# Performance work log

Hardware: AMD Instinct MI355X
Metric: run time of the kernel (lower is better)

The kernel has to match this reference:

```python
import jax, jax.numpy as jnp
import numpy as np

B, S_NEW, DIM = 32, 1, 4096
H, KV, HD = 32, 8, 128          # query heads, kv heads, head_dim
PREV = 2048                      # tokens already in the KV cache


def setup_inputs() -> dict:
    key = jax.random.key(0)
    ks = jax.random.split(key, 8)
    return {
        "x": jax.random.normal(ks[0], (B, S_NEW, DIM), jnp.float32),
        "wq": jax.random.normal(ks[1], (DIM, H * HD), jnp.float32) * 0.02,
        "wk": jax.random.normal(ks[2], (DIM, KV * HD), jnp.float32) * 0.02,
        "wv": jax.random.normal(ks[3], (DIM, KV * HD), jnp.float32) * 0.02,
        "wo": jax.random.normal(ks[4], (H * HD, DIM), jnp.float32) * 0.02,
        "cache_k": jax.random.normal(ks[5], (B, PREV, KV, HD), jnp.float32),
        "cache_v": jax.random.normal(ks[6], (B, PREV, KV, HD), jnp.float32),
        "freqs": jax.random.normal(ks[7], (S_NEW, HD // 2), jnp.float32),  # rotary angles (angle of freqs_cis)
    }


def _apply_rope(t, cos, sin):
    # t: [b, s, h, hd]; interleaved pairs as in torch.view_as_complex
    a = t[..., 0::2]
    b = t[..., 1::2]
    c = cos[None, :, None, :]
    s = sin[None, :, None, :]
    ra = a * c - b * s
    rb = a * s + b * c
    return jnp.stack([ra, rb], axis=-1).reshape(t.shape)


def reference(x, wq, wk, wv, wo, cache_k, cache_v, freqs):
    b, s, _ = x.shape  # s == 1 (decode)
    xq = (x @ wq).reshape(b, s, H, HD)
    xk = (x @ wk).reshape(b, s, KV, HD)
    xv = (x @ wv).reshape(b, s, KV, HD)

    cos, sin = jnp.cos(freqs), jnp.sin(freqs)
    xq = _apply_rope(xq, cos, sin)
    xk = _apply_rope(xk, cos, sin)

    # KV-cache append (update_cache_decode)
    k_full = jnp.concatenate([cache_k, xk], axis=1)  # [b, PREV+1, KV, hd]
    v_full = jnp.concatenate([cache_v, xv], axis=1)

    # GQA attention without materializing the expanded cache
    g = H // KV
    q = xq.reshape(b, KV, g, HD)  # s == 1 folded away
    scale = 1.0 / jnp.sqrt(jnp.asarray(HD, x.dtype))
    scores = jnp.einsum("bkgd,bskd->bkgs", q, k_full) * scale  # [b, KV, g, PREV+1]
    attn = jax.nn.softmax(scores, axis=-1)
    out = jnp.einsum("bkgs,bskd->bkgd", attn, v_full)  # [b, KV, g, hd]
    out = out.reshape(b, s, H * HD)
    return out @ wo
```

## Files before the change

kernel.cpp:

```cpp
#include <hip/hip_runtime.h>


#define WS_P1   0
#define WS_QKV  6291456
#define WS_ATTN 6488064
#define WS_P2   6619136
#define WS_SC   10813440
#define WS_LINV 12914688
#define WS_PA   12915712

__global__ __launch_bounds__(256) void gemm_skinny(
    const float* __restrict__ X,
    const float* __restrict__ W0, int e0, int ld0,
    const float* __restrict__ W1, int e1, int ld1,
    const float* __restrict__ W2, int ld2,
    float* __restrict__ P, int Ntot)
{
    __shared__ float x_t[128][36];
    __shared__ float2 red[128][33];

    const int nb = blockIdx.x * 256;
    const float* W; int ld, noff;
    if (nb < e0)      { W = W0; ld = ld0; noff = 0;  }
    else if (nb < e1) { W = W1; ld = ld1; noff = e0; }
    else              { W = W2; ld = ld2; noff = e1; }

    const int k0  = blockIdx.y * 128;
    const int tid = threadIdx.x;
    const int cp  = tid & 127;
    const int kg  = tid >> 7;
    const int nn  = nb - noff + cp * 2;

    #pragma unroll
    for (int i = 0; i < 16; ++i) {
        int idx = tid + i * 256;
        int bb = idx >> 7, kk = idx & 127;
        x_t[kk][bb] = X[(size_t)bb * 4096 + k0 + kk];
    }
    __syncthreads();

    float2 acc[32];
    #pragma unroll
    for (int b = 0; b < 32; ++b) { acc[b].x = 0.f; acc[b].y = 0.f; }

    const float* Wp = W + (size_t)k0 * ld + nn;
    for (int kk0 = kg * 64; kk0 < kg * 64 + 64; kk0 += 8) {
        float2 w[8];
        #pragma unroll
        for (int u = 0; u < 8; ++u)
            w[u] = *(const float2*)&Wp[(size_t)(kk0 + u) * ld];
        #pragma unroll
        for (int u = 0; u < 8; ++u) {
            const float* xr = x_t[kk0 + u];
            #pragma unroll
            for (int bq = 0; bq < 8; ++bq) {
                float4 xv = *(const float4*)&xr[bq * 4];
                acc[bq*4+0].x += xv.x * w[u].x; acc[bq*4+0].y += xv.x * w[u].y;
                acc[bq*4+1].x += xv.y * w[u].x; acc[bq*4+1].y += xv.y * w[u].y;
                acc[bq*4+2].x += xv.z * w[u].x; acc[bq*4+2].y += xv.z * w[u].y;
                acc[bq*4+3].x += xv.w * w[u].x; acc[bq*4+3].y += xv.w * w[u].y;
            }
        }
    }

    if (kg == 1) {
        #pragma unroll
        for (int b = 0; b < 32; ++b) red[cp][b] = acc[b];
    }
    __syncthreads();
    if (kg == 0) {
        const int ks = blockIdx.y;
        #pragma unroll
        for (int b = 0; b < 32; ++b) {
            float2 o = red[cp][b];
            float2 v; v.x = acc[b].x + o.x; v.y = acc[b].y + o.y;
            *(float2*)&P[((size_t)ks * 32 + b) * Ntot + nb + cp * 2] = v;
        }
    }
}

__global__ __launch_bounds__(128) void reduce_rope(
    const float* __restrict__ P, const float* __restrict__ freqs,
    float* __restrict__ qkv)
{
    int t = blockIdx.x * 128 + threadIdx.x;
    int b = t / 3072;
    int cp = t - b * 3072;
    int n = cp * 2;
    float sx = 0.f, sy = 0.f;
    #pragma unroll
    for (int ks = 0; ks < 32; ++ks) {
        float2 v = *(const float2*)&P[((size_t)ks * 32 + b) * 6144 + n];
        sx += v.x; sy += v.y;
    }
    if (n < 5120) {
        int d = n & 127;
        float fr = freqs[d >> 1];
        float c = cosf(fr), s = sinf(fr);
        float ra = sx * c - sy * s;
        float rb = sx * s + sy * c;
        if (n < 4096) {
            const float sc = 0.08838834764831845f;
            ra *= sc; rb *= sc;
        }
        sx = ra; sy = rb;
    }
    float2 o; o.x = sx; o.y = sy;
    *(float2*)&qkv[(size_t)b * 6144 + n] = o;
}

__global__ __launch_bounds__(256) void attn_scores(
    const float* __restrict__ qkv,
    const float* __restrict__ ck,
    float* __restrict__ sc)
{
    const int blk = blockIdx.x;
    const int c   = blk & 15;
    const int kv  = (blk >> 4) & 7;
    const int b   = blk >> 7;
    const int tid = threadIdx.x;
    const int wave = tid >> 6, lane = tid & 63;
    const int psub = (lane >> 4) & 3, dl = lane & 15;
    const int s0 = c * 128;

    float q[4][8];
    {
        const float* qb = qkv + (size_t)b * 6144 + kv * 512 + dl * 8;
        #pragma unroll
        for (int h = 0; h < 4; ++h) {
            float4 a = *(const float4*)&qb[h * 128];
            float4 e = *(const float4*)&qb[h * 128 + 4];
            q[h][0]=a.x; q[h][1]=a.y; q[h][2]=a.z; q[h][3]=a.w;
            q[h][4]=e.x; q[h][5]=e.y; q[h][6]=e.z; q[h][7]=e.w;
        }
    }

    float* scb = sc + (size_t)(b * 8 + kv) * 8208;
    const float* kbase = ck + (((size_t)b * 2048 + s0) * 8 + kv) * 128;
    const int srow = wave * 4 + psub;

    for (int it0 = 0; it0 < 8; it0 += 2) {
        float4 kA[2][2];
        #pragma unroll
        for (int u = 0; u < 2; ++u) {
            const float* kr = kbase + (size_t)((it0 + u) * 16 + srow) * 1024 + dl * 8;
            kA[u][0] = *(const float4*)kr;
            kA[u][1] = *(const float4*)(kr + 4);
        }
        #pragma unroll
        for (int u = 0; u < 2; ++u) {
            float p[4];
            #pragma unroll
            for (int h = 0; h < 4; ++h) {
                p[h] = q[h][0]*kA[u][0].x + q[h][1]*kA[u][0].y
                     + q[h][2]*kA[u][0].z + q[h][3]*kA[u][0].w
                     + q[h][4]*kA[u][1].x + q[h][5]*kA[u][1].y
                     + q[h][6]*kA[u][1].z + q[h][7]*kA[u][1].w;
            }
            #pragma unroll
            for (int off = 1; off < 16; off <<= 1) {
                #pragma unroll
                for (int h = 0; h < 4; ++h) p[h] += __shfl_xor(p[h], off);
            }
            if (dl == 0) {
                int s = s0 + (it0 + u) * 16 + srow;
                float4 o; o.x = p[0]; o.y = p[1]; o.z = p[2]; o.w = p[3];
                *(float4*)&scb[(size_t)s * 4] = o;
            }
        }
    }

    if (c == 15 && wave == 0 && psub == 0) {
        const float* kr = qkv + (size_t)b * 6144 + 4096 + kv * 128 + dl * 8;
        float4 k0 = *(const float4*)kr;
        float4 k1 = *(const float4*)(kr + 4);
        float p[4];
        #pragma unroll
        for (int h = 0; h < 4; ++h) {
            p[h] = q[h][0]*k0.x + q[h][1]*k0.y + q[h][2]*k0.z + q[h][3]*k0.w
                 + q[h][4]*k1.x + q[h][5]*k1.y + q[h][6]*k1.z + q[h][7]*k1.w;
        }
        #pragma unroll
        for (int off = 1; off < 16; off <<= 1) {
            #pragma unroll
            for (int h = 0; h < 4; ++h) p[h] += __shfl_xor(p[h], off);
        }
        if (dl == 0) {
            float4 o; o.x = p[0]; o.y = p[1]; o.z = p[2]; o.w = p[3];
            *(float4*)&scb[(size_t)2048 * 4] = o;
        }
    }
}

__global__ __launch_bounds__(256) void attn_softmax(
    float* __restrict__ sc, float* __restrict__ linv)
{
    __shared__ float red[4][4];
    const int g = blockIdx.x;
    float* scb = sc + (size_t)g * 8208;
    const int tid = threadIdx.x;
    const int wave = tid >> 6, lane = tid & 63;

    float4 m4; m4.x = -1e30f; m4.y = -1e30f; m4.z = -1e30f; m4.w = -1e30f;
    for (int s = tid; s < 2049; s += 256) {
        float4 v = *(const float4*)&scb[(size_t)s * 4];
        m4.x = fmaxf(m4.x, v.x); m4.y = fmaxf(m4.y, v.y);
        m4.z = fmaxf(m4.z, v.z); m4.w = fmaxf(m4.w, v.w);
    }
    #pragma unroll
    for (int off = 1; off < 64; off <<= 1) {
        m4.x = fmaxf(m4.x, __shfl_xor(m4.x, off));
        m4.y = fmaxf(m4.y, __shfl_xor(m4.y, off));
        m4.z = fmaxf(m4.z, __shfl_xor(m4.z, off));
        m4.w = fmaxf(m4.w, __shfl_xor(m4.w, off));
    }
    if (lane == 0) {
        red[wave][0] = m4.x; red[wave][1] = m4.y;
        red[wave][2] = m4.z; red[wave][3] = m4.w;
    }
    __syncthreads();
    float4 M;
    M.x = fmaxf(fmaxf(red[0][0], red[1][0]), fmaxf(red[2][0], red[3][0]));
    M.y = fmaxf(fmaxf(red[0][1], red[1][1]), fmaxf(red[2][1], red[3][1]));
    M.z = fmaxf(fmaxf(red[0][2], red[1][2]), fmaxf(red[2][2], red[3][2]));
    M.w = fmaxf(fmaxf(red[0][3], red[1][3]), fmaxf(red[2][3], red[3][3]));
    __syncthreads();

    float4 l4; l4.x = 0.f; l4.y = 0.f; l4.z = 0.f; l4.w = 0.f;
    for (int s = tid; s < 2049; s += 256) {
        float4 v = *(const float4*)&scb[(size_t)s * 4];
        v.x = __expf(v.x - M.x); v.y = __expf(v.y - M.y);
        v.z = __expf(v.z - M.z); v.w = __expf(v.w - M.w);
        *(float4*)&scb[(size_t)s * 4] = v;
        l4.x += v.x; l4.y += v.y; l4.z += v.z; l4.w += v.w;
    }
    #pragma unroll
    for (int off = 1; off < 64; off <<= 1) {
        l4.x += __shfl_xor(l4.x, off);
        l4.y += __shfl_xor(l4.y, off);
        l4.z += __shfl_xor(l4.z, off);
        l4.w += __shfl_xor(l4.w, off);
    }
    if (lane == 0) {
        red[wave][0] = l4.x; red[wave][1] = l4.y;
        red[wave][2] = l4.z; red[wave][3] = l4.w;
    }
    __syncthreads();
    if (tid < 4) {
        float L = red[0][tid] + red[1][tid] + red[2][tid] + red[3][tid];
        linv[(size_t)g * 4 + tid] = 1.0f / L;
    }
}

__global__ __launch_bounds__(256) void attn_pv(
    const float* __restrict__ qkv, const float* __restrict__ cv,
    const float* __restrict__ sc, const float* __restrict__ linv,
    float* __restrict__ pa)
{
    __shared__ float sbuf[8][512];
    const int blk = blockIdx.x;
    const int c   = blk & 7;
    const int kv  = (blk >> 3) & 7;
    const int b   = blk >> 6;
    const int tid = threadIdx.x;
    const int grp = tid >> 5, l32 = tid & 31, d4 = l32 * 4;
    const int s0 = c * 256;

    const float* scb = sc + (size_t)(b * 8 + kv) * 8208;
    const float* vbase = cv + (((size_t)b * 2048 + s0) * 8 + kv) * 128;

    float4 acc[4];
    #pragma unroll
    for (int h = 0; h < 4; ++h) { acc[h].x=0.f; acc[h].y=0.f; acc[h].z=0.f; acc[h].w=0.f; }

    for (int it = 0; it < 8; ++it) {
        float4 vv[4];
        float4 pj[4];
        #pragma unroll
        for (int j = 0; j < 4; ++j) {
            int sl = it * 32 + j * 8 + grp;
            vv[j] = *(const float4*)&vbase[(size_t)sl * 1024 + d4];
        }
        #pragma unroll
        for (int j = 0; j < 4; ++j) {
            int sl = it * 32 + j * 8 + grp;
            pj[j] = *(const float4*)&scb[(size_t)(s0 + sl) * 4];
        }
        #pragma unroll
        for (int j = 0; j < 4; ++j) {
            acc[0].x += pj[j].x * vv[j].x; acc[0].y += pj[j].x * vv[j].y;
            acc[0].z += pj[j].x * vv[j].z; acc[0].w += pj[j].x * vv[j].w;
            acc[1].x += pj[j].y * vv[j].x; acc[1].y += pj[j].y * vv[j].y;
            acc[1].z += pj[j].y * vv[j].z; acc[1].w += pj[j].y * vv[j].w;
            acc[2].x += pj[j].z * vv[j].x; acc[2].y += pj[j].z * vv[j].y;
            acc[2].z += pj[j].z * vv[j].z; acc[2].w += pj[j].z * vv[j].w;
            acc[3].x += pj[j].w * vv[j].x; acc[3].y += pj[j].w * vv[j].y;
            acc[3].z += pj[j].w * vv[j].z; acc[3].w += pj[j].w * vv[j].w;
        }
    }
    if (c == 7 && grp == 0) {
        const float* vr = qkv + (size_t)b * 6144 + 5120 + kv * 128;
        float4 v = *(const float4*)&vr[d4];
        float4 p = *(const float4*)&scb[(size_t)2048 * 4];
        acc[0].x += p.x * v.x; acc[0].y += p.x * v.y; acc[0].z += p.x * v.z; acc[0].w += p.x * v.w;
        acc[1].x += p.y * v.x; acc[1].y += p.y * v.y; acc[1].z += p.y * v.z; acc[1].w += p.y * v.w;
        acc[2].x += p.z * v.x; acc[2].y += p.z * v.y; acc[2].z += p.z * v.z; acc[2].w += p.z * v.w;
        acc[3].x += p.w * v.x; acc[3].y += p.w * v.y; acc[3].z += p.w * v.z; acc[3].w += p.w * v.w;
    }

    {
        float4 li = *(const float4*)&linv[(size_t)(b * 8 + kv) * 4];
        acc[0].x *= li.x; acc[0].y *= li.x; acc[0].z *= li.x; acc[0].w *= li.x;
        acc[1].x *= li.y; acc[1].y *= li.y; acc[1].z *= li.y; acc[1].w *= li.y;
        acc[2].x *= li.z; acc[2].y *= li.z; acc[2].z *= li.z; acc[2].w *= li.z;
        acc[3].x *= li.w; acc[3].y *= li.w; acc[3].z *= li.w; acc[3].w *= li.w;
    }
    #pragma unroll
    for (int h = 0; h < 4; ++h)
        *(float4*)&sbuf[grp][h * 128 + d4] = acc[h];
    __syncthreads();

    float* rec = pa + (size_t)blk * 512;
    for (int t = tid; t < 512; t += 256) {
        float v = 0.f;
        #pragma unroll
        for (int g2 = 0; g2 < 8; ++g2) v += sbuf[g2][t];
        rec[t] = v;
    }
}

__global__ __launch_bounds__(128) void attn_combine(
    const float* __restrict__ pa, float* __restrict__ ao)
{
    const int g = blockIdx.x;
    const int d = threadIdx.x;
    const float* base = pa + (size_t)g * 8 * 512;
    #pragma unroll
    for (int h = 0; h < 4; ++h) {
        float v = 0.f;
        #pragma unroll
        for (int c = 0; c < 8; ++c) v += base[c * 512 + h * 128 + d];
        ao[(size_t)(g >> 3) * 4096 + (g & 7) * 512 + h * 128 + d] = v;
    }
}

__global__ __launch_bounds__(128) void reduce_out(
    const float* __restrict__ P, float* __restrict__ out)
{
    int t = blockIdx.x * 128 + threadIdx.x;
    int b = t >> 11;
    int cp = t & 2047;
    int n = cp * 2;
    float sx = 0.f, sy = 0.f;
    #pragma unroll
    for (int ks = 0; ks < 32; ++ks) {
        float2 v = *(const float2*)&P[((size_t)ks * 32 + b) * 4096 + n];
        sx += v.x; sy += v.y;
    }
    float2 o; o.x = sx; o.y = sy;
    *(float2*)&out[(size_t)b * 4096 + n] = o;
}

extern "C" void kernel_launch(void* const* d_in, const int* in_sizes, int n_in,
                              void* d_out, int out_size, void* d_ws, size_t ws_size,
                              hipStream_t stream) {
    const float* x  = (const float*)d_in[0];
    const float* wq = (const float*)d_in[1];
    const float* wk = (const float*)d_in[2];
    const float* wv = (const float*)d_in[3];
    const float* wo = (const float*)d_in[4];
    const float* ck = (const float*)d_in[5];
    const float* cv = (const float*)d_in[6];
    const float* fr = (const float*)d_in[7];
    float* out = (float*)d_out;
    float* ws  = (float*)d_ws;

    float* P1   = ws + WS_P1;
    float* qkv  = ws + WS_QKV;
    float* attn = ws + WS_ATTN;
    float* P2   = ws + WS_P2;
    float* SC   = ws + WS_SC;
    float* LINV = ws + WS_LINV;
    float* PA   = ws + WS_PA;

    dim3 g1(24, 32);
    gemm_skinny<<<g1, 256, 0, stream>>>(x, wq, 4096, 4096, wk, 5120, 1024,
                                        wv, 1024, P1, 6144);
    reduce_rope<<<768, 128, 0, stream>>>(P1, fr, qkv);
    attn_scores<<<4096, 256, 0, stream>>>(qkv, ck, SC);
    attn_softmax<<<256, 256, 0, stream>>>(SC, LINV);
    attn_pv<<<2048, 256, 0, stream>>>(qkv, cv, SC, LINV, PA);
    attn_combine<<<256, 128, 0, stream>>>(PA, attn);
    dim3 g4(16, 32);
    gemm_skinny<<<g4, 256, 0, stream>>>(attn, wo, 4096, 4096, wo, 4096, 4096,
                                        wo, 4096, P2, 4096);
    reduce_out<<<512, 128, 0, stream>>>(P2, out);
}
```

Baseline: 207.3 us.

## Cover all KV heads per block in attention scores and PV over contiguous rows

attn_scores and attn_pv now give each block 32 contiguous sequence rows across all 8 KV heads, instead of one KV head over a longer span. Each block therefore streams full 4 KB cache rows contiguously. The score buffer becomes a per-batch interleaved [s][kv][4] layout, and softmax is adapted to read it. The PV partials grow to 64 chunks of 4096 floats per batch, and a rewritten combine kernel reduces them. This adds extra workspace traffic and footprint in exchange for more contiguous cache reads.

Measured after the change: 247.3 us. +19.3%, slower.

```diff
diff --git a/kernel.cpp b/kernel.cpp
--- a/kernel.cpp
+++ b/kernel.cpp
@@ -110,84 +110,78 @@
 }
 
 __global__ __launch_bounds__(256) void attn_scores(
-    const float* __restrict__ qkv,
-    const float* __restrict__ ck,
+    const float* __restrict__ qkv, const float* __restrict__ ck,
     float* __restrict__ sc)
 {
     const int blk = blockIdx.x;
-    const int c   = blk & 15;
-    const int kv  = (blk >> 4) & 7;
-    const int b   = blk >> 7;
-    const int tid = threadIdx.x;
-    const int wave = tid >> 6, lane = tid & 63;
-    const int psub = (lane >> 4) & 3, dl = lane & 15;
-    const int s0 = c * 128;
-
-    float q[4][8];
+    const int c = blk & 63;
+    const int b = blk >> 6;
+    const int t = threadIdx.x;
+    const int jj = t & 15;
+    const int kv = (t >> 4) & 7;
+    const int tm = t >> 7;
+
+    float4 q[4][2];
     {
-        const float* qb = qkv + (size_t)b * 6144 + kv * 512 + dl * 8;
+        const float* qb = qkv + (size_t)b * 6144 + (kv * 4) * 128 + jj * 8;
         #pragma unroll
         for (int h = 0; h < 4; ++h) {
-            float4 a = *(const float4*)&qb[h * 128];
-            float4 e = *(const float4*)&qb[h * 128 + 4];
-            q[h][0]=a.x; q[h][1]=a.y; q[h][2]=a.z; q[h][3]=a.w;
-            q[h][4]=e.x; q[h][5]=e.y; q[h][6]=e.z; q[h][7]=e.w;
-        }
-    }
-
-    float* scb = sc + (size_t)(b * 8 + kv) * 8208;
-    const float* kbase = ck + (((size_t)b * 2048 + s0) * 8 + kv) * 128;
-    const int srow = wave * 4 + psub;
-
-    for (int it0 = 0; it0 < 8; it0 += 2) {
-        float4 kA[2][2];
+            q[h][0] = *(const float4*)(qb + h * 128);
+            q[h][1] = *(const float4*)(qb + h * 128 + 4);
+        }
+    }
+
+    const int r0 = c * 32 + tm * 16;
+    const float* kbase = ck + ((size_t)b * 2048 + r0) * 1024 + kv * 128 + jj * 8;
+    float* scb = sc + (size_t)b * 65664;
+
+    for (int r = 0; r < 16; r += 2) {
+        float4 ka[2][2];
         #pragma unroll
         for (int u = 0; u < 2; ++u) {
-            const float* kr = kbase + (size_t)((it0 + u) * 16 + srow) * 1024 + dl * 8;
-            kA[u][0] = *(const float4*)kr;
-            kA[u][1] = *(const float4*)(kr + 4);
+            ka[u][0] = *(const float4*)(kbase + (size_t)(r + u) * 1024);
+            ka[u][1] = *(const float4*)(kbase + (size_t)(r + u) * 1024 + 4);
         }
         #pragma unroll
         for (int u = 0; u < 2; ++u) {
             float p[4];
             #pragma unroll
             for (int h = 0; h < 4; ++h) {
-                p[h] = q[h][0]*kA[u][0].x + q[h][1]*kA[u][0].y
-                     + q[h][2]*kA[u][0].z + q[h][3]*kA[u][0].w
-                     + q[h][4]*kA[u][1].x + q[h][5]*kA[u][1].y
-                     + q[h][6]*kA[u][1].z + q[h][7]*kA[u][1].w;
+                p[h] = q[h][0].x*ka[u][0].x + q[h][0].y*ka[u][0].y
+                     + q[h][0].z*ka[u][0].z + q[h][0].w*ka[u][0].w
+                     + q[h][1].x*ka[u][1].x + q[h][1].y*ka[u][1].y
+                     + q[h][1].z*ka[u][1].z + q[h][1].w*ka[u][1].w;
             }
             #pragma unroll
             for (int off = 1; off < 16; off <<= 1) {
                 #pragma unroll
                 for (int h = 0; h < 4; ++h) p[h] += __shfl_xor(p[h], off);
             }
-            if (dl == 0) {
-                int s = s0 + (it0 + u) * 16 + srow;
+            if (jj == 0) {
                 float4 o; o.x = p[0]; o.y = p[1]; o.z = p[2]; o.w = p[3];
-                *(float4*)&scb[(size_t)s * 4] = o;
+                *(float4*)&scb[(size_t)(r0 + r + u) * 32 + kv * 4] = o;
             }
         }
     }
 
-    if (c == 15 && wave == 0 && psub == 0) {
-        const float* kr = qkv + (size_t)b * 6144 + 4096 + kv * 128 + dl * 8;
+    if (c == 63 && tm == 1) {
+        const float* kr = qkv + (size_t)b * 6144 + 4096 + kv * 128 + jj * 8;
         float4 k0 = *(const float4*)kr;
         float4 k1 = *(const float4*)(kr + 4);
         float p[4];
         #pragma unroll
         for (int h = 0; h < 4; ++h) {
-            p[h] = q[h][0]*k0.x + q[h][1]*k0.y + q[h][2]*k0.z + q[h][3]*k0.w
-                 + q[h][4]*k1.x + q[h][5]*k1.y + q[h][6]*k1.z + q[h][7]*k1.w;
+            p[h] = q[h][0].x*k0.x + q[h][0].y*k0.y + q[h][0].z*k0.z + q[h][0].w*k0.w
+                 + q[h][1].x*k1.x + q[h][1].y*k1.y + q[h][1].z*k1.z + q[h][1].w*k1.w;
         }
         #pragma unroll
         for (int off = 1; off < 16; off <<= 1) {
             #pragma unroll
             for (int h = 0; h < 4; ++h) p[h] += __shfl_xor(p[h], off);
         }
-        if (dl == 0) {
+        if (jj == 0) {
             float4 o; o.x = p[0]; o.y = p[1]; o.z = p[2]; o.w = p[3];
-            *(float4*)&scb[(size_t)2048 * 4] = o;
+            *(float4*)&scb[(size_t)2048 * 32 + kv * 4] = o;
         }
     }
 }
@@ -197,13 +191,14 @@
 {
     __shared__ float red[4][4];
     const int g = blockIdx.x;
-    float* scb = sc + (size_t)g * 8208;
+    const int b = g >> 3, kv = g & 7;
+    float* scb = sc + (size_t)b * 65664 + kv * 4;
     const int tid = threadIdx.x;
     const int wave = tid >> 6, lane = tid & 63;
 
     float4 m4; m4.x = -1e30f; m4.y = -1e30f; m4.z = -1e30f; m4.w = -1e30f;
     for (int s = tid; s < 2049; s += 256) {
-        float4 v = *(const float4*)&scb[(size_t)s * 4];
+        float4 v = *(const float4*)&scb[(size_t)s * 32];
         m4.x = fmaxf(m4.x, v.x); m4.y = fmaxf(m4.y, v.y);
         m4.z = fmaxf(m4.z, v.z); m4.w = fmaxf(m4.w, v.w);
     }
@@ -228,10 +223,10 @@
 
     float4 l4; l4.x = 0.f; l4.y = 0.f; l4.z = 0.f; l4.w = 0.f;
     for (int s = tid; s < 2049; s += 256) {
-        float4 v = *(const float4*)&scb[(size_t)s * 4];
+        float4 v = *(const float4*)&scb[(size_t)s * 32];
         v.x = __expf(v.x - M.x); v.y = __expf(v.y - M.y);
         v.z = __expf(v.z - M.z); v.w = __expf(v.w - M.w);
-        *(float4*)&scb[(size_t)s * 4] = v;
+        *(float4*)&scb[(size_t)s * 32] = v;
         l4.x += v.x; l4.y += v.y; l4.z += v.z; l4.w += v.w;
     }
     #pragma unroll
@@ -257,91 +252,123 @@
     const float* __restrict__ sc, const float* __restrict__ linv,
     float* __restrict__ pa)
 {
-    __shared__ float sbuf[8][512];
+    __shared__ float sbuf[128 * 33];
     const int blk = blockIdx.x;
-    const int c   = blk & 7;
-    const int kv  = (blk >> 3) & 7;
-    const int b   = blk >> 6;
-    const int tid = threadIdx.x;
-    const int grp = tid >> 5, l32 = tid & 31, d4 = l32 * 4;
-    const int s0 = c * 256;
-
-    const float* scb = sc + (size_t)(b * 8 + kv) * 8208;
-    const float* vbase = cv + (((size_t)b * 2048 + s0) * 8 + kv) * 128;
-
-    float4 acc[4];
-    #pragma unroll
-    for (int h = 0; h < 4; ++h) { acc[h].x=0.f; acc[h].y=0.f; acc[h].z=0.f; acc[h].w=0.f; }
-
-    for (int it = 0; it < 8; ++it) {
-        float4 vv[4];
-        float4 pj[4];
-        #pragma unroll
-        for (int j = 0; j < 4; ++j) {
-            int sl = it * 32 + j * 8 + grp;
-            vv[j] = *(const float4*)&vbase[(size_t)sl * 1024 + d4];
-        }
-        #pragma unroll
-        for (int j = 0; j < 4; ++j) {
-            int sl = it * 32 + j * 8 + grp;
-            pj[j] = *(const float4*)&scb[(size_t)(s0 + sl) * 4];
-        }
-        #pragma unroll
-        for (int j = 0; j < 4; ++j) {
-            acc[0].x += pj[j].x * vv[j].x; acc[0].y += pj[j].x * vv[j].y;
-            acc[0].z += pj[j].x * vv[j].z; acc[0].w += pj[j].x * vv[j].w;
-            acc[1].x += pj[j].y * vv[j].x; acc[1].y += pj[j].y * vv[j].y;
-            acc[1].z += pj[j].y * vv[j].z; acc[1].w += pj[j].y * vv[j].w;
-            acc[2].x += pj[j].z * vv[j].x; acc[2].y += pj[j].z * vv[j].y;
-            acc[2].z += pj[j].z * vv[j].z; acc[2].w += pj[j].z * vv[j].w;
-            acc[3].x += pj[j].w * vv[j].x; acc[3].y += pj[j].w * vv[j].y;
-            acc[3].z += pj[j].w * vv[j].z; acc[3].w += pj[j].w * vv[j].w;
-        }
-    }
-    if (c == 7 && grp == 0) {
-        const float* vr = qkv + (size_t)b * 6144 + 5120 + kv * 128;
-        float4 v = *(const float4*)&vr[d4];
-        float4 p = *(const float4*)&scb[(size_t)2048 * 4];
-        acc[0].x += p.x * v.x; acc[0].y += p.x * v.y; acc[0].z += p.x * v.z; acc[0].w += p.x * v.w;
-        acc[1].x += p.y * v.x; acc[1].y += p.y * v.y; acc[1].z += p.y * v.z; acc[1].w += p.y * v.w;
-        acc[2].x += p.z * v.x; acc[2].y += p.z * v.y; acc[2].z += p.z * v.z; acc[2].w += p.z * v.w;
-        acc[3].x += p.w * v.x; acc[3].y += p.w * v.y; acc[3].z += p.w * v.z; acc[3].w += p.w * v.w;
+    const int c = blk & 63;
+    const int b = blk >> 6;
+    const int t = threadIdx.x;
+    const int jj = t & 15;
+    const int kv = (t >> 4) & 7;
+    const int tm = t >> 7;
+
+    float4 acc[4][2];
+    #pragma unroll
+    for (int h = 0; h < 4; ++h) {
+        #pragma unroll
+        for (int u = 0; u < 2; ++u) { acc[h][u].x=0.f; acc[h][u].y=0.f; acc[h][u].z=0.f; acc[h][u].w=0.f; }
+    }
+
+    const int r0 = c * 32 + tm * 16;
+    const float* vbase = cv + ((size_t)b * 2048 + r0) * 1024 + kv * 128 + jj * 8;
+    const float* scb = sc + (size_t)b * 65664 + kv * 4;
+
+    for (int r = 0; r < 16; r += 2) {
+        float4 va[2][2];
+        float4 p4[2];
+        #pragma unroll
+        for (int u = 0; u < 2; ++u) {
+            va[u][0] = *(const float4*)(vbase + (size_t)(r + u) * 1024);
+            va[u][1] = *(const float4*)(vbase + (size_t)(r + u) * 1024 + 4);
+            p4[u] = *(const float4*)&scb[(size_t)(r0 + r + u) * 32];
+        }
+        #pragma unroll
+        for (int u = 0; u < 2; ++u) {
+            acc[0][0].x += p4[u].x*va[u][0].x; acc[0][0].y += p4[u].x*va[u][0].y;
+            acc[0][0].z += p4[u].x*va[u][0].z; acc[0][0].w += p4[u].x*va[u][0].w;
+            acc[0][1].x += p4[u].x*va[u][1].x; acc[0][1].y += p4[u].x*va[u][1].y;
+            acc[0][1].z += p4[u].x*va[u][1].z; acc[0][1].w += p4[u].x*va[u][1].w;
+            acc[1][0].x += p4[u].y*va[u][0].x; acc[1][0].y += p4[u].y*va[u][0].y;
+            acc[1][0].z += p4[u].y*va[u][0].z; acc[1][0].w += p4[u].y*va[u][0].w;
+            acc[1][1].x += p4[u].y*va[u][1].x; acc[1][1].y += p4[u].y*va[u][1].y;
+            acc[1][1].z += p4[u].y*va[u][1].z; acc[1][1].w += p4[u].y*va[u][1].w;
+            acc[2][0].x += p4[u].z*va[u][0].x; acc[2][0].y += p4[u].z*va[u][0].y;
+            acc[2][0].z += p4[u].z*va[u][0].z; acc[2][0].w += p4[u].z*va[u][0].w;
+            acc[2][1].x += p4[u].z*va[u][1].x; acc[2][1].y += p4[u].z*va[u][1].y;
+            acc[2][1].z += p4[u].z*va[u][1].z; acc[2][1].w += p4[u].z*va[u][1].w;
+            acc[3][0].x += p4[u].w*va[u][0].x; acc[3][0].y += p4[u].w*va[u][0].y;
+            acc[3][0].z += p4[u].w*va[u][0].z; acc[3][0].w += p4[u].w*va[u][0].w;
+            acc[3][1].x += p4[u].w*va[u][1].x; acc[3][1].y += p4[u].w*va[u][1].y;
+            acc[3][1].z += p4[u].w*va[u][1].z; acc[3][1].w += p4[u].w*va[u][1].w;
+        }
+    }
+
+    if (c == 63 && tm == 1) {
+        const float* vr = qkv + (size_t)b * 6144 + 5120 + kv * 128 + jj * 8;
+        float4 v0 = *(const float4*)vr;
+        float4 v1 = *(const float4*)(vr + 4);
+        float4 p = *(const float4*)&scb[(size_t)2048 * 32];
+        acc[0][0].x += p.x*v0.x; acc[0][0].y += p.x*v0.y; acc[0][0].z += p.x*v0.z; acc[0][0].w += p.x*v0.w;
+        acc[0][1].x += p.x*v1.x; acc[0][1].y += p.x*v1.y; acc[0][1].z += p.x*v1.z; acc[0][1].w += p.x*v1.w;
+        acc[1][0].x += p.y*v0.x; acc[1][0].y += p.y*v0.y; acc[1][0].z += p.y*v0.z; acc[1][0].w += p.y*v0.w;
+        acc[1][1].x += p.y*v1.x; acc[1][1].y += p.y*v1.y; acc[1][1].z += p.y*v1.z; acc[1][1].w += p.y*v1.w;
+        acc[2][0].x += p.z*v0.x; acc[2][0].y += p.z*v0.y; acc[2][0].z += p.z*v0.z; acc[2][0].w += p.z*v0.w;
+        acc[2][1].x += p.z*v1.x; acc[2][1].y += p.z*v1.y; acc[2][1].z += p.z*v1.z; acc[2][1].w += p.z*v1.w;
+        acc[3][0].x += p.w*v0.x; acc[3][0].y += p.w*v0.y; acc[3][0].z += p.w*v0.z; acc[3][0].w += p.w*v0.w;
+        acc[3][1].x += p.w*v1.x; acc[3][1].y += p.w*v1.y; acc[3][1].z += p.w*v1.z; acc[3][1].w += p.w*v1.w;
     }
 
     {
-        float4 li = *(const float4*)&linv[(size_t)(b * 8 + kv) * 4];
-        acc[0].x *= li.x; acc[0].y *= li.x; acc[0].z *= li.x; acc[0].w *= li.x;
-        acc[1].x *= li.y; acc[1].y *= li.y; acc[1].z *= li.y; acc[1].w *= li.y;
-        acc[2].x *= li.z; acc[2].y *= li.z; acc[2].z *= li.z; acc[2].w *= li.z;
-        acc[3].x *= li.w; acc[3].y *= li.w; acc[3].z *= li.w; acc[3].w *= li.w;
-    }
-    #pragma unroll
-    for (int h = 0; h < 4; ++h)
-        *(float4*)&sbuf[grp][h * 128 + d4] = acc[h];
-    __syncthreads();
-
-    float* rec = pa + (size_t)blk * 512;
-    for (int t = tid; t < 512; t += 256) {
-        float v = 0.f;
-        #pragma unroll
-        for (int g2 = 0; g2 < 8; ++g2) v += sbuf[g2][t];
-        rec[t] = v;
-    }
-}
-
-__global__ __launch_bounds__(128) void attn_combine(
+        float4 li = *(const float4*)&linv[(size_t)((b * 8 + kv) * 4)];
+        #pragma unroll
+        for (int u = 0; u < 2; ++u) {
+            acc[0][u].x *= li.x; acc[0][u].y *= li.x; acc[0][u].z *= li.x; acc[0][u].w *= li.x;
+            acc[1][u].x *= li.y; acc[1][u].y *= li.y; acc[1][u].z *= li.y; acc[1][u].w *= li.y;
+            acc[2][u].x *= li.z; acc[2][u].y *= li.z; acc[2][u].z *= li.z; acc[2][u].w *= li.z;
+            acc[3][u].x *= li.w; acc[3][u].y *= li.w; acc[3][u].z *= li.w; acc[3][u].w *= li.w;
+        }
+    }
+
+    if (tm == 1) {
+        const int li_ = t - 128;
+        float* d = &sbuf[li_ * 33];
+        #pragma unroll
+        for (int h = 0; h < 4; ++h) {
+            d[h*8+0] = acc[h][0].x; d[h*8+1] = acc[h][0].y;
+            d[h*8+2] = acc[h][0].z; d[h*8+3] = acc[h][0].w;
+            d[h*8+4] = acc[h][1].x; d[h*8+5] = acc[h][1].y;
+            d[h*8+6] = acc[h][1].z; d[h*8+7] = acc[h][1].w;
+        }
+    }
+    __syncthreads();
+    if (tm == 0) {
+        const float* s_ = &sbuf[t * 33];
+        #pragma unroll
+        for (int h = 0; h < 4; ++h) {
+            acc[h][0].x += s_[h*8+0]; acc[h][0].y += s_[h*8+1];
+            acc[h][0].z += s_[h*8+2]; acc[h][0].w += s_[h*8+3];
+            acc[h][1].x += s_[h*8+4]; acc[h][1].y += s_[h*8+5];
+            acc[h][1].z += s_[h*8+6]; acc[h][1].w += s_[h*8+7];
+        }
+        float* rec = pa + (size_t)blk * 4096 + (kv * 4) * 128 + jj * 8;
+        #pragma unroll
+        for (int h = 0; h < 4; ++h) {
+            *(float4*)(rec + h * 128)     = acc[h][0];
+            *(float4*)(rec + h * 128 + 4) = acc[h][1];
+        }
+    }
+}
+
+__global__ __launch_bounds__(256) void attn_combine(
     const float* __restrict__ pa, float* __restrict__ ao)
 {
-    const int g = blockIdx.x;
-    const int d = threadIdx.x;
-    const float* base = pa + (size_t)g * 8 * 512;
-    #pragma unroll
-    for (int h = 0; h < 4; ++h) {
-        float v = 0.f;
-        #pragma unroll
-        for (int c = 0; c < 8; ++c) v += base[c * 512 + h * 128 + d];
-        ao[(size_t)(g >> 3) * 4096 + (g & 7) * 512 + h * 128 + d] = v;
-    }
+    const int blk = blockIdx.x;
+    const int b = blk >> 4, seg = blk & 15;
+    const int j = seg * 256 + threadIdx.x;
+    const float* base = pa + (size_t)b * 64 * 4096 + j;
+    float v = 0.f;
+    #pragma unroll 8
+    for (int c2 = 0; c2 < 64; ++c2) v += base[(size_t)c2 * 4096];
+    ao[(size_t)b * 4096 + j] = v;
 }
 
 __global__ __launch_bounds__(128) void reduce_out(
@@ -387,10 +414,10 @@
     gemm_skinny<<<g1, 256, 0, stream>>>(x, wq, 4096, 4096, wk, 5120, 1024,
                                         wv, 1024, P1, 6144);
     reduce_rope<<<768, 128, 0, stream>>>(P1, fr, qkv);
-    attn_scores<<<4096, 256, 0, stream>>>(qkv, ck, SC);
+    attn_scores<<<2048, 256, 0, stream>>>(qkv, ck, SC);
     attn_softmax<<<256, 256, 0, stream>>>(SC, LINV);
     attn_pv<<<2048, 256, 0, stream>>>(qkv, cv, SC, LINV, PA);
-    attn_combine<<<256, 128, 0, stream>>>(PA, attn);
+    attn_combine<<<512, 256, 0, stream>>>(PA, attn);
     dim3 g4(16, 32);
     gemm_skinny<<<g4, 256, 0, stream>>>(attn, wo, 4096, 4096, wo, 4096, 4096,
                                         wo, 4096, P2, 4096);
```
